# Kernel optimization log

Measured on AMD Instinct MI355X. Metric: run time of the kernel, lower is better.

## Reference

```python
import jax, jax.numpy as jnp
import numpy as np

TEMPERATURE = 0.1
NEG_INF = -1e30


def setup_inputs() -> dict:
    key = jax.random.key(0)
    kf, kl = jax.random.split(key)
    N, D = 8192, 128
    features = jax.random.normal(kf, (N, D), dtype=jnp.float32)
    # labels in [-1, 80): -1 marks background rows that are filtered out
    labels = jax.random.randint(kl, (N,), -1, 80)
    return {"features": features, "labels": labels}


def reference(features, labels):
    N = labels.shape[0]
    fg = labels >= 0  # [N]

    # F.normalize(p=2, dim=1): x / max(||x||, eps)
    norm = jnp.maximum(jnp.linalg.norm(features, axis=1, keepdims=True), 1e-12)
    f = features / norm

    sim = jnp.matmul(f, f.T) / TEMPERATURE  # [N, N]

    pair_fg = fg[:, None] & fg[None, :]
    eye = jnp.eye(N, dtype=bool)
    label_eq = labels[:, None] == labels[None, :]
    pos_mask = pair_fg & label_eq & ~eye          # positives (same label, not self)
    all_mask = pair_fg & ~eye                     # pos | neg == everything but self (within fg)

    # row-wise masked max, clamped to [-20, 20] as in the original
    max_sim = jnp.max(jnp.where(all_mask, sim, NEG_INF), axis=1)
    max_sim = jnp.clip(max_sim, -20.0, 20.0)

    e = jnp.exp(sim - max_sim[:, None])           # cos-sim/temp is bounded, no overflow
    pos_sum = jnp.clip(jnp.sum(jnp.where(pos_mask, e, 0.0), axis=1), 1e-6, 1e6)
    all_sum = jnp.clip(jnp.sum(jnp.where(all_mask, e, 0.0), axis=1), 1e-6, 1e6)

    loss_i = jnp.minimum(-jnp.log(pos_sum / all_sum), 10.0)  # clamp(max=10)

    # rows contributing to the mean: fg rows with at least one positive
    valid = fg & (jnp.sum(pos_mask, axis=1) > 0)
    n_valid = jnp.sum(valid)
    mean_loss = jnp.sum(jnp.where(valid, loss_i, 0.0)) / jnp.maximum(n_valid, 1).astype(jnp.float32)

    ok = (jnp.sum(fg) >= 2) & (n_valid > 0)
    return jnp.where(ok, mean_loss, jnp.float32(0.0))
```

## Files before the change

### kernel.cpp

```cpp
#include <hip/hip_runtime.h>

#define N 8192
#define D 128
#define CHUNK 512
#define NCC (N / CHUNK)
#define NBIN 81
#define PBLK 512

typedef unsigned short u16;
typedef __attribute__((ext_vector_type(8))) __bf16 bf16x8;
typedef __attribute__((ext_vector_type(4))) float f32x4;

#define PREP_SCALE 3.7982889979f

__device__ __forceinline__ u16 f2bf(float x) {
  unsigned u = __float_as_uint(x);
  u += 0x7fff + ((u >> 16) & 1);
  return (u16)(u >> 16);
}

__global__ __launch_bounds__(256) void cpe_prep(const float* __restrict__ feat,
                                                const int* __restrict__ labels,
                                                u16* __restrict__ fhi,
                                                int* __restrict__ slab,
                                                float* __restrict__ acc3) {
  __shared__ int hist[4][NBIN], part[4][NBIN], lbase[NBIN], lpos[16];
  const int tid = threadIdx.x;
  const int w = tid >> 6, l = tid & 63;
  const int bid = blockIdx.x;
  if (tid < NBIN) {
#pragma unroll
    for (int cp = 0; cp < 4; ++cp) { hist[cp][tid] = 0; part[cp][tid] = 0; }
  }
  if (bid == 0 && tid < 4) acc3[tid] = 0.0f;
  __syncthreads();
  const int myBase = bid * 16;
  for (int j = tid; j < N; j += 256) {
    const int lab = labels[j] + 1;
    atomicAdd(&hist[w][lab], 1);
    if (j < myBase) atomicAdd(&part[w][lab], 1);
  }
  __syncthreads();
  if (tid < NBIN) {
    hist[0][tid] += hist[1][tid] + hist[2][tid] + hist[3][tid];
    part[0][tid] += part[1][tid] + part[2][tid] + part[3][tid];
  }
  __syncthreads();
  if (tid == 0) {
    int s = 0;
    for (int b = 0; b < NBIN; ++b) { lbase[b] = s; s += hist[0][b]; }
  }
  __syncthreads();
  if (tid < 16) {
    const int L = labels[myBase + tid] + 1;
    int pos = lbase[L] + part[0][L];
    for (int k = 0; k < tid; ++k) pos += (labels[myBase + k] + 1 == L) ? 1 : 0;
    lpos[tid] = pos;
    slab[pos] = L - 1;
  }
  __syncthreads();
#pragma unroll
  for (int rr = 0; rr < 4; ++rr) {
    const int k = w * 4 + rr;
    const float2 x = *(const float2*)&feat[(myBase + k) * D + l * 2];
    float s = x.x * x.x + x.y * x.y;
#pragma unroll
    for (int sh = 1; sh < 64; sh <<= 1) s += __shfl_xor(s, sh);
    const float inv = PREP_SCALE / fmaxf(sqrtf(s), 1e-12f);
    const int pos = lpos[k];
    *(ushort2*)&fhi[pos * D + l * 2] = make_ushort2(f2bf(x.x * inv), f2bf(x.y * inv));
  }
}

__global__ __launch_bounds__(256, 2) void cpe_main(
    const u16* __restrict__ fhi, const int* __restrict__ slab,
    float2* __restrict__ partials) {
  __shared__ int Lab[CHUNK];
  const int rt = blockIdx.x, cc = blockIdx.y;
  const int tid = threadIdx.x;
  const int w = tid >> 6, l = tid & 63, q = l >> 4, m = l & 15;
  const int r0w = rt * 256 + w * 64;
  const int cbase0 = cc * CHUNK;

  Lab[tid] = slab[cbase0 + tid];
  Lab[tid + 256] = slab[cbase0 + 256 + tid];

  const int labi_lo = slab[r0w], labi_hi = slab[r0w + 63];

  bf16x8 Ah[4][4];
  int labi[4][4];
#pragma unroll
  for (int tr = 0; tr < 4; ++tr) {
    const int row = r0w + tr * 16 + m;
#pragma unroll
    for (int ks = 0; ks < 4; ++ks)
      Ah[tr][ks] = *(const bf16x8*)&fhi[row * D + ks * 32 + q * 8];
#pragma unroll
    for (int v = 0; v < 4; ++v) labi[tr][v] = slab[r0w + tr * 16 + q * 4 + v];
  }

  float ps[4][4], as_[4][4];
#pragma unroll
  for (int tr = 0; tr < 4; ++tr)
#pragma unroll
    for (int v = 0; v < 4; ++v) { ps[tr][v] = 0.f; as_[tr][v] = 0.f; }

  __syncthreads();

  for (int jt = 0; jt < CHUNK / 16; ++jt) {
    const int tb = jt * 16;
    const int labj_lo = Lab[tb], labj_hi = Lab[tb + 15];
    if (labj_hi < 0) continue;
    const bool slow = (labj_lo < 0) | ((labj_hi >= labi_lo) & (labj_lo <= labi_hi));
    const int jrow = cbase0 + tb + m;
    f32x4 acc[4];
#pragma unroll
    for (int tr = 0; tr < 4; ++tr) acc[tr] = (f32x4){0.f, 0.f, 0.f, 0.f};
#pragma unroll
    for (int ks = 0; ks < 4; ++ks) {
      const bf16x8 bh = *(const bf16x8*)&fhi[(size_t)jrow * D + ks * 32 + q * 8];
#pragma unroll
      for (int tr = 0; tr < 4; ++tr)
        acc[tr] = __builtin_amdgcn_mfma_f32_16x16x32_bf16(Ah[tr][ks], bh, acc[tr], 0, 0, 0);
    }
    if (!slow) {
#pragma unroll
      for (int tr = 0; tr < 4; ++tr)
#pragma unroll
        for (int v = 0; v < 4; ++v)
          as_[tr][v] += __builtin_amdgcn_exp2f(acc[tr][v]);
    } else {
      const int labj = Lab[tb + m];
      const bool fgj = labj >= 0;
      const int jbase = cbase0 + tb;
#pragma unroll
      for (int tr = 0; tr < 4; ++tr) {
        if (jbase == r0w + tr * 16) {
#pragma unroll
          for (int v = 0; v < 4; ++v) {
            const float e = __builtin_amdgcn_exp2f(acc[tr][v]);
            const float em = (fgj && (m != q * 4 + v)) ? e : 0.0f;
            as_[tr][v] += em;
            ps[tr][v] += (labj == labi[tr][v]) ? em : 0.0f;
          }
        } else {
#pragma unroll
          for (int v = 0; v < 4; ++v) {
            const float e = __builtin_amdgcn_exp2f(acc[tr][v]);
            const float em = fgj ? e : 0.0f;
            as_[tr][v] += em;
            ps[tr][v] += (labj == labi[tr][v]) ? em : 0.0f;
          }
        }
      }
    }
  }

#pragma unroll
  for (int tr = 0; tr < 4; ++tr)
#pragma unroll
    for (int v = 0; v < 4; ++v) {
      float vp = ps[tr][v], va = as_[tr][v];
#pragma unroll
      for (int s = 1; s < 16; s <<= 1) {
        vp += __shfl_xor(vp, s);
        va += __shfl_xor(va, s);
      }
      if (m == 0)
        partials[(size_t)cc * N + r0w + tr * 16 + q * 4 + v] = make_float2(vp, va);
    }
}

__global__ __launch_bounds__(256) void cpe_rows(const float2* __restrict__ partials,
                                                const int* __restrict__ slab,
                                                float* __restrict__ acc3,
                                                float* __restrict__ out) {
  const int r = blockIdx.x * 256 + threadIdx.x;
  float psr = 0.f, asr = 0.f;
#pragma unroll
  for (int c = 0; c < NCC; ++c) {
    const float2 p = partials[(size_t)c * N + r];
    psr += p.x;
    asr += p.y;
  }
  const bool fg = slab[r] >= 0;
  const bool valid = fg && (psr > 0.f);
  const float loss = fminf(logf(asr / psr), 10.0f);
  float v0 = valid ? loss : 0.f;
  float v1 = valid ? 1.f : 0.f;
  float v2 = fg ? 1.f : 0.f;
#pragma unroll
  for (int s = 1; s < 64; s <<= 1) {
    v0 += __shfl_xor(v0, s);
    v1 += __shfl_xor(v1, s);
    v2 += __shfl_xor(v2, s);
  }
  __shared__ float red[3][4];
  const int w = threadIdx.x >> 6, l = threadIdx.x & 63;
  if (l == 0) { red[0][w] = v0; red[1][w] = v1; red[2][w] = v2; }
  __syncthreads();
  if (threadIdx.x == 0) {
    atomicAdd(&acc3[0], red[0][0] + red[0][1] + red[0][2] + red[0][3]);
    atomicAdd(&acc3[1], red[1][0] + red[1][1] + red[1][2] + red[1][3]);
    atomicAdd(&acc3[2], red[2][0] + red[2][1] + red[2][2] + red[2][3]);
    __threadfence();
    const unsigned old = atomicAdd((unsigned*)&acc3[3], 1u);
    if (old == gridDim.x - 1) {
      const float ls = atomicAdd(&acc3[0], 0.0f);
      const float nv = atomicAdd(&acc3[1], 0.0f);
      const float nf = atomicAdd(&acc3[2], 0.0f);
      out[0] = (nf >= 2.0f && nv > 0.0f) ? ls / fmaxf(nv, 1.0f) : 0.0f;
    }
  }
}

extern "C" void kernel_launch(void* const* d_in, const int* in_sizes, int n_in,
                              void* d_out, int out_size, void* d_ws, size_t ws_size,
                              hipStream_t stream) {
  const float* feat = (const float*)d_in[0];
  const int* labels = (const int*)d_in[1];
  float* out = (float*)d_out;
  char* ws = (char*)d_ws;
  u16* fhi = (u16*)ws;
  float2* partials = (float2*)(ws + (size_t)N * D * 2);
  char* tail = ws + (size_t)N * D * 2 + (size_t)NCC * N * 8;
  int* slab = (int*)tail;
  float* acc3 = (float*)(tail + N * 4);

  cpe_prep<<<PBLK, 256, 0, stream>>>(feat, labels, fhi, slab, acc3);
  cpe_main<<<dim3(N / 256, NCC), 256, 0, stream>>>(fhi, slab, partials);
  cpe_rows<<<N / 256, 256, 0, stream>>>(partials, slab, acc3, out);
}
```

Measured before the change: 112.2 us.

## Halve column chunk, skip background rows/columns, and prefetch next B tile

Column chunk size drops from 512 to 256, doubling the grid's column dimension so more blocks run. The prep kernel now records how many rows are background after label sorting. The main kernel uses that count to start each chunk's column loop past the background columns and to skip row tiles that are all background. The B-operand loads are software-pipelined one tile ahead, and row labels move from registers into shared memory. This lowers register pressure but adds LDS reads in the slow path and doubles the partials written and reduced.

After: 121.1 us. 1.08x slower.

```diff
diff --git a/kernel.cpp b/kernel.cpp
--- a/kernel.cpp
+++ b/kernel.cpp
@@ -2,7 +2,8 @@
 
 #define N 8192
 #define D 128
-#define CHUNK 512
+#define CHUNK 256
+#define NT (CHUNK / 16)
 #define NCC (N / CHUNK)
 #define NBIN 81
 #define PBLK 512
@@ -23,7 +24,8 @@
                                                 const int* __restrict__ labels,
                                                 u16* __restrict__ fhi,
                                                 int* __restrict__ slab,
-                                                float* __restrict__ acc3) {
+                                                float* __restrict__ acc3,
+                                                int* __restrict__ nbgp) {
   __shared__ int hist[4][NBIN], part[4][NBIN], lbase[NBIN], lpos[16];
   const int tid = threadIdx.x;
   const int w = tid >> 6, l = tid & 63;
@@ -49,6 +51,7 @@
   if (tid == 0) {
     int s = 0;
     for (int b = 0; b < NBIN; ++b) { lbase[b] = s; s += hist[0][b]; }
+    if (bid == 0) *nbgp = lbase[1];
   }
   __syncthreads();
   if (tid < 16) {
@@ -74,8 +77,9 @@
 
 __global__ __launch_bounds__(256, 2) void cpe_main(
     const u16* __restrict__ fhi, const int* __restrict__ slab,
-    float2* __restrict__ partials) {
+    const int* __restrict__ nbgp, float2* __restrict__ partials) {
   __shared__ int Lab[CHUNK];
+  __shared__ int LabI[256];
   const int rt = blockIdx.x, cc = blockIdx.y;
   const int tid = threadIdx.x;
   const int w = tid >> 6, l = tid & 63, q = l >> 4, m = l & 15;
@@ -83,20 +87,18 @@
   const int cbase0 = cc * CHUNK;
 
   Lab[tid] = slab[cbase0 + tid];
-  Lab[tid + 256] = slab[cbase0 + 256 + tid];
+  LabI[tid] = slab[rt * 256 + tid];
 
   const int labi_lo = slab[r0w], labi_hi = slab[r0w + 63];
+  const int nbg = *nbgp;
 
   bf16x8 Ah[4][4];
-  int labi[4][4];
 #pragma unroll
   for (int tr = 0; tr < 4; ++tr) {
     const int row = r0w + tr * 16 + m;
 #pragma unroll
     for (int ks = 0; ks < 4; ++ks)
       Ah[tr][ks] = *(const bf16x8*)&fhi[row * D + ks * 32 + q * 8];
-#pragma unroll
-    for (int v = 0; v < 4; ++v) labi[tr][v] = slab[r0w + tr * 16 + q * 4 + v];
   }
 
   float ps[4][4], as_[4][4];
@@ -107,52 +109,70 @@
 
   __syncthreads();
 
-  for (int jt = 0; jt < CHUNK / 16; ++jt) {
-    const int tb = jt * 16;
-    const int labj_lo = Lab[tb], labj_hi = Lab[tb + 15];
-    if (labj_hi < 0) continue;
-    const bool slow = (labj_lo < 0) | ((labj_hi >= labi_lo) & (labj_lo <= labi_hi));
-    const int jrow = cbase0 + tb + m;
-    f32x4 acc[4];
-#pragma unroll
-    for (int tr = 0; tr < 4; ++tr) acc[tr] = (f32x4){0.f, 0.f, 0.f, 0.f};
-#pragma unroll
-    for (int ks = 0; ks < 4; ++ks) {
-      const bf16x8 bh = *(const bf16x8*)&fhi[(size_t)jrow * D + ks * 32 + q * 8];
-#pragma unroll
-      for (int tr = 0; tr < 4; ++tr)
-        acc[tr] = __builtin_amdgcn_mfma_f32_16x16x32_bf16(Ah[tr][ks], bh, acc[tr], 0, 0, 0);
-    }
-    if (!slow) {
-#pragma unroll
-      for (int tr = 0; tr < 4; ++tr)
-#pragma unroll
-        for (int v = 0; v < 4; ++v)
-          as_[tr][v] += __builtin_amdgcn_exp2f(acc[tr][v]);
-    } else {
-      const int labj = Lab[tb + m];
-      const bool fgj = labj >= 0;
-      const int jbase = cbase0 + tb;
+  const int nb = nbg - cbase0;
+  const int jt_lo = (nb < 16) ? 0 : ((nb >> 4) < NT ? (nb >> 4) : NT);
+
+  if (labi_hi >= 0 && jt_lo < NT) {
+    const u16* bp = &fhi[(size_t)(cbase0 + jt_lo * 16 + m) * D + q * 8];
+    bf16x8 b0 = *(const bf16x8*)&bp[0];
+    bf16x8 b1 = *(const bf16x8*)&bp[32];
+    bf16x8 b2 = *(const bf16x8*)&bp[64];
+    bf16x8 b3 = *(const bf16x8*)&bp[96];
+
+    for (int jt = jt_lo; jt < NT; ++jt) {
+      const int tb = jt * 16;
+      const int jn = (jt + 1 < NT) ? jt + 1 : jt;
+      const u16* np = &fhi[(size_t)(cbase0 + jn * 16 + m) * D + q * 8];
+      const bf16x8 n0 = *(const bf16x8*)&np[0];
+      const bf16x8 n1 = *(const bf16x8*)&np[32];
+      const bf16x8 n2 = *(const bf16x8*)&np[64];
+      const bf16x8 n3 = *(const bf16x8*)&np[96];
+
+      f32x4 acc[4];
+#pragma unroll
+      for (int tr = 0; tr < 4; ++tr) acc[tr] = (f32x4){0.f, 0.f, 0.f, 0.f};
 #pragma unroll
       for (int tr = 0; tr < 4; ++tr) {
-        if (jbase == r0w + tr * 16) {
-#pragma unroll
-          for (int v = 0; v < 4; ++v) {
-            const float e = __builtin_amdgcn_exp2f(acc[tr][v]);
-            const float em = (fgj && (m != q * 4 + v)) ? e : 0.0f;
-            as_[tr][v] += em;
-            ps[tr][v] += (labj == labi[tr][v]) ? em : 0.0f;
-          }
-        } else {
-#pragma unroll
-          for (int v = 0; v < 4; ++v) {
-            const float e = __builtin_amdgcn_exp2f(acc[tr][v]);
-            const float em = fgj ? e : 0.0f;
-            as_[tr][v] += em;
-            ps[tr][v] += (labj == labi[tr][v]) ? em : 0.0f;
+        acc[tr] = __builtin_amdgcn_mfma_f32_16x16x32_bf16(Ah[tr][0], b0, acc[tr], 0, 0, 0);
+        acc[tr] = __builtin_amdgcn_mfma_f32_16x16x32_bf16(Ah[tr][1], b1, acc[tr], 0, 0, 0);
+        acc[tr] = __builtin_amdgcn_mfma_f32_16x16x32_bf16(Ah[tr][2], b2, acc[tr], 0, 0, 0);
+        acc[tr] = __builtin_amdgcn_mfma_f32_16x16x32_bf16(Ah[tr][3], b3, acc[tr], 0, 0, 0);
+      }
+
+      const int labj_lo = Lab[tb], labj_hi = Lab[tb + 15];
+      const bool slow = (labj_lo < 0) | ((labj_hi >= labi_lo) & (labj_lo <= labi_hi));
+      if (!slow) {
+#pragma unroll
+        for (int tr = 0; tr < 4; ++tr)
+#pragma unroll
+          for (int v = 0; v < 4; ++v)
+            as_[tr][v] += __builtin_amdgcn_exp2f(acc[tr][v]);
+      } else {
+        const int labj = Lab[tb + m];
+        const bool fgj = labj >= 0;
+        const int jbase = cbase0 + tb;
+#pragma unroll
+        for (int tr = 0; tr < 4; ++tr) {
+          if (jbase == r0w + tr * 16) {
+#pragma unroll
+            for (int v = 0; v < 4; ++v) {
+              const float e = __builtin_amdgcn_exp2f(acc[tr][v]);
+              const float em = (fgj && (m != q * 4 + v)) ? e : 0.0f;
+              as_[tr][v] += em;
+              ps[tr][v] += (labj == LabI[w * 64 + tr * 16 + q * 4 + v]) ? em : 0.0f;
+            }
+          } else {
+#pragma unroll
+            for (int v = 0; v < 4; ++v) {
+              const float e = __builtin_amdgcn_exp2f(acc[tr][v]);
+              const float em = fgj ? e : 0.0f;
+              as_[tr][v] += em;
+              ps[tr][v] += (labj == LabI[w * 64 + tr * 16 + q * 4 + v]) ? em : 0.0f;
+            }
           }
         }
       }
+      b0 = n0; b1 = n1; b2 = n2; b3 = n3;
     }
   }
 
@@ -226,8 +246,9 @@
   char* tail = ws + (size_t)N * D * 2 + (size_t)NCC * N * 8;
   int* slab = (int*)tail;
   float* acc3 = (float*)(tail + N * 4);
-
-  cpe_prep<<<PBLK, 256, 0, stream>>>(feat, labels, fhi, slab, acc3);
-  cpe_main<<<dim3(N / 256, NCC), 256, 0, stream>>>(fhi, slab, partials);
+  int* nbgp = (int*)(tail + N * 4 + 64);
+
+  cpe_prep<<<PBLK, 256, 0, stream>>>(feat, labels, fhi, slab, acc3, nbgp);
+  cpe_main<<<dim3(N / 256, NCC), 256, 0, stream>>>(fhi, slab, nbgp, partials);
   cpe_rows<<<N / 256, 256, 0, stream>>>(partials, slab, acc3, out);
 }
```
